# Performance work log

Hardware: AMD Instinct MI355X
Metric: run time of the kernel (lower is better)

## Reference

```python
import jax, jax.numpy as jnp
import numpy as np

LEAKY_SLOPE = 0.01  # torch F.leaky_relu default
COS_EPS = 1e-8      # torch F.cosine_similarity default eps


def _gc(pre, cur, adj, W):
    # GraphConvolution.forward
    pre_w = pre @ W            # [N, d]
    cur_w = cur @ W            # [M, d]
    new_pre = adj @ cur_w      # [N, d]
    new_cur = adj.T @ pre_w    # [M, d]
    new_pre = jnp.where(new_pre >= 0, new_pre, LEAKY_SLOPE * new_pre)
    new_cur = jnp.where(new_cur >= 0, new_cur, LEAKY_SLOPE * new_cur)
    return new_pre, new_cur


def _cos_sim(pre, cur):
    # Fused pairwise cosine similarity: matches torch F.cosine_similarity per pair
    dots = pre @ cur.T                         # [N, M]
    n_pre = jnp.linalg.norm(pre, axis=1)       # [N]
    n_cur = jnp.linalg.norm(cur, axis=1)       # [M]
    denom = jnp.maximum(n_pre[:, None] * n_cur[None, :], COS_EPS)
    return dots / denom


def setup_inputs() -> dict:
    key = jax.random.key(0)
    k1, k2, k3, k4, k5 = jax.random.split(key, 5)
    N, d = 8192, 128
    stdv = 1.0 / np.sqrt(d)
    pre = jax.random.normal(k1, (N, d), dtype=jnp.float32)
    cur = jax.random.normal(k2, (N, d), dtype=jnp.float32)
    adj = jax.random.uniform(k3, (N, N), dtype=jnp.float32)
    W1 = jax.random.uniform(k4, (d, d), dtype=jnp.float32, minval=-stdv, maxval=stdv)
    W2 = jax.random.uniform(k5, (d, d), dtype=jnp.float32, minval=-stdv, maxval=stdv)
    return {"pre": pre, "cur": cur, "adj": adj, "W1": W1, "W2": W2}


def reference(pre, cur, adj, W1, W2):
    pre1, cur1 = _gc(pre, cur, adj, W1)
    adj1 = _cos_sim(pre1, cur1)
    pre2, cur2 = _gc(pre1, cur1, adj1, W2)
    adj2 = _cos_sim(pre2, cur2)
    return adj2
```

## Files before the change

kernel.cpp:

```cpp
#include <hip/hip_runtime.h>


#define NN 8192
#define DD 128

typedef __bf16 bf16x8 __attribute__((ext_vector_type(8)));
typedef float f32x4 __attribute__((ext_vector_type(4)));

static __device__ __forceinline__ float4 ldg4(const float* p) {
    return *reinterpret_cast<const float4*>(p);
}

static __device__ __forceinline__ unsigned f2bf2(float lo, float hi) {
    __bf16 a = (__bf16)lo, b = (__bf16)hi;
    unsigned short ua = __builtin_bit_cast(unsigned short, a);
    unsigned short ub = __builtin_bit_cast(unsigned short, b);
    return (unsigned)ua | ((unsigned)ub << 16);
}

static __device__ __forceinline__ int swz16(int row) {
    return (((row & 7) ^ ((row >> 3) & 7)) << 4);
}

template<int AMODE>
__global__ __launch_bounds__(256, 4)
void mfma_tn(const void* __restrict__ Aptr, int lda,
             const unsigned short* __restrict__ BTa,
             const unsigned short* __restrict__ BTb, int ldbt,
             float* __restrict__ C, int ldc,
             int ksplit, int zstride)
{
    __shared__ alignas(16) char smem[34816];
    char* smA = smem;
    char* smB = smem + 16384;

    const int t    = threadIdx.x;
    const int l    = t & 63;
    const int w    = t >> 6;
    const int wr   = (w >> 1) * 64;
    const int wc   = (w & 1) * 64;
    const int lrow = l & 15;
    const int lhi  = l >> 4;
    const int i0   = blockIdx.x * 128;
    const int j0   = blockIdx.y * 128;
    const int z    = blockIdx.z;
    const bool second = (AMODE == 3) && (z >= 8);
    const unsigned short* BT = second ? BTb : BTa;
    const int kbase = (AMODE == 3) ? (z & 7) * ksplit : 0;
    C += (size_t)z * (size_t)zstride;

    const int srow = t >> 3;
    const int skg  = t & 7;
    const int u    = t & 31;
    const int r8   = t >> 5;

    f32x4 acc[4][4];
    #pragma unroll
    for (int r = 0; r < 4; ++r)
        #pragma unroll
        for (int q = 0; q < 4; ++q)
            #pragma unroll
            for (int e = 0; e < 4; ++e) acc[r][q][e] = 0.0f;

    for (int k0 = 0; k0 < ksplit; k0 += 64) {
        const int kk = kbase + k0;

        if (AMODE == 3 && second) {
            const float* gA = (const float*)Aptr;
            float4 rv[8];
            #pragma unroll
            for (int e = 0; e < 8; ++e)
                rv[e] = ldg4(&gA[(size_t)(kk + r8 * 8 + e) * lda + i0 + u * 4]);
            {
                int c = u * 4;
                uint4 wv;
                wv.x = f2bf2(rv[0].x, rv[1].x); wv.y = f2bf2(rv[2].x, rv[3].x);
                wv.z = f2bf2(rv[4].x, rv[5].x); wv.w = f2bf2(rv[6].x, rv[7].x);
                *reinterpret_cast<uint4*>(smA + c * 128 + ((r8 << 4) ^ swz16(c))) = wv;
                c = u * 4 + 1;
                wv.x = f2bf2(rv[0].y, rv[1].y); wv.y = f2bf2(rv[2].y, rv[3].y);
                wv.z = f2bf2(rv[4].y, rv[5].y); wv.w = f2bf2(rv[6].y, rv[7].y);
                *reinterpret_cast<uint4*>(smA + c * 128 + ((r8 << 4) ^ swz16(c))) = wv;
                c = u * 4 + 2;
                wv.x = f2bf2(rv[0].z, rv[1].z); wv.y = f2bf2(rv[2].z, rv[3].z);
                wv.z = f2bf2(rv[4].z, rv[5].z); wv.w = f2bf2(rv[6].z, rv[7].z);
                *reinterpret_cast<uint4*>(smA + c * 128 + ((r8 << 4) ^ swz16(c))) = wv;
                c = u * 4 + 3;
                wv.x = f2bf2(rv[0].w, rv[1].w); wv.y = f2bf2(rv[2].w, rv[3].w);
                wv.z = f2bf2(rv[4].w, rv[5].w); wv.w = f2bf2(rv[6].w, rv[7].w);
                *reinterpret_cast<uint4*>(smA + c * 128 + ((r8 << 4) ^ swz16(c))) = wv;
            }
        } else {
            #pragma unroll
            for (int it = 0; it < 4; ++it) {
                const int row = it * 32 + srow;
                const int dst = row * 128 + ((skg << 4) ^ swz16(row));
                if constexpr (AMODE == 3) {
                    const float* g = (const float*)Aptr + (size_t)(i0 + row) * lda + kk + skg * 8;
                    float4 f0 = ldg4(g), f1 = ldg4(g + 4);
                    uint4 wv;
                    wv.x = f2bf2(f0.x, f0.y);
                    wv.y = f2bf2(f0.z, f0.w);
                    wv.z = f2bf2(f1.x, f1.y);
                    wv.w = f2bf2(f1.z, f1.w);
                    *reinterpret_cast<uint4*>(smA + dst) = wv;
                } else {
                    const unsigned short* g = (const unsigned short*)Aptr + (size_t)(i0 + row) * lda + kk + skg * 8;
                    *reinterpret_cast<uint4*>(smA + dst) = *reinterpret_cast<const uint4*>(g);
                }
            }
        }

        #pragma unroll
        for (int it = 0; it < 4; ++it) {
            const int row = it * 32 + srow;
            const int dst = row * 128 + ((skg << 4) ^ swz16(row));
            const unsigned short* gb = BT + (size_t)(j0 + it * 32 + srow) * ldbt + kk + skg * 8;
            *reinterpret_cast<uint4*>(smB + dst) = *reinterpret_cast<const uint4*>(gb);
        }
        __syncthreads();

        #pragma unroll
        for (int s = 0; s < 2; ++s) {
            bf16x8 af[4], bq[4];
            #pragma unroll
            for (int r = 0; r < 4; ++r) {
                const int row = wr + r * 16 + lrow;
                af[r] = *reinterpret_cast<const bf16x8*>(
                    smA + row * 128 + ((s * 64 + lhi * 16) ^ swz16(row)));
            }
            #pragma unroll
            for (int q = 0; q < 4; ++q) {
                const int col = wc + q * 16 + lrow;
                bq[q] = *reinterpret_cast<const bf16x8*>(
                    smB + col * 128 + ((s * 64 + lhi * 16) ^ swz16(col)));
            }
            #pragma unroll
            for (int r = 0; r < 4; ++r)
                #pragma unroll
                for (int q = 0; q < 4; ++q)
                    acc[r][q] = __builtin_amdgcn_mfma_f32_16x16x32_bf16(af[r], bq[q], acc[r][q], 0, 0, 0);
        }
        __syncthreads();
    }

    float* sC = (float*)smem;
    #pragma unroll
    for (int h = 0; h < 2; ++h) {
        if ((w & 1) == h) {
            #pragma unroll
            for (int r = 0; r < 4; ++r)
                #pragma unroll
                for (int q = 0; q < 4; ++q)
                    #pragma unroll
                    for (int i = 0; i < 4; ++i)
                        sC[(wr + r * 16 + lhi * 4 + i) * 68 + q * 16 + lrow] = acc[r][q][i];
        }
        __syncthreads();
        #pragma unroll
        for (int it = 0; it < 8; ++it) {
            const int idx = it * 256 + t;
            const int row = idx >> 4;
            const int c4  = (idx & 15) << 2;
            f32x4 v = *reinterpret_cast<const f32x4*>(&sC[row * 68 + c4]);
            float* dst = &C[(size_t)(i0 + row) * ldc + j0 + h * 64 + c4];
            if constexpr (AMODE == 0)
                __builtin_nontemporal_store(v, reinterpret_cast<f32x4*>(dst));
            else
                *reinterpret_cast<f32x4*>(dst) = v;
        }
        __syncthreads();
    }
}

__global__ __launch_bounds__(256, 2)
void gemm_w1t(const float* __restrict__ pre, const float* __restrict__ cur,
              const float* __restrict__ W1,
              unsigned short* __restrict__ pwT, unsigned short* __restrict__ cwT)
{
    __shared__ float sA[32][68];
    __shared__ float sB[64][128];

    const int t  = threadIdx.x;
    const int ct = t & 31;
    const int rt = t >> 5;
    const int bx = blockIdx.x;
    const bool isCur = bx >= 256;
    const float* A = isCur ? cur : pre;
    unsigned short* XT = isCur ? cwT : pwT;
    const int i0 = (bx & 255) * 32;

    float4 acc[4];
    #pragma unroll
    for (int r = 0; r < 4; ++r) { acc[r].x = 0.f; acc[r].y = 0.f; acc[r].z = 0.f; acc[r].w = 0.f; }

    for (int k0 = 0; k0 < DD; k0 += 64) {
        #pragma unroll
        for (int f = 0; f < 2; ++f) {
            const int row = (t >> 4) + 16 * f;
            const int kk4 = (t & 15) << 2;
            *reinterpret_cast<float4*>(&sA[row][kk4]) =
                ldg4(&A[(size_t)(i0 + row) * DD + k0 + kk4]);
        }
        #pragma unroll
        for (int f = 0; f < 8; ++f) {
            const int idx = f * 256 + t;
            const int kk  = idx >> 5;
            const int c4  = (idx & 31) << 2;
            *reinterpret_cast<float4*>(&sB[kk][c4]) =
                ldg4(&W1[(size_t)(k0 + kk) * DD + c4]);
        }
        __syncthreads();
        #pragma unroll 4
        for (int kk = 0; kk < 64; kk += 4) {
            float4 a[4], b[4];
            #pragma unroll
            for (int r = 0; r < 4; ++r)
                a[r] = *reinterpret_cast<const float4*>(&sA[rt * 4 + r][kk]);
            #pragma unroll
            for (int q = 0; q < 4; ++q)
                b[q] = *reinterpret_cast<const float4*>(&sB[kk + q][ct * 4]);
            #pragma unroll
            for (int r = 0; r < 4; ++r) {
                acc[r].x += a[r].x * b[0].x; acc[r].y += a[r].x * b[0].y;
                acc[r].z += a[r].x * b[0].z; acc[r].w += a[r].x * b[0].w;
                acc[r].x += a[r].y * b[1].x; acc[r].y += a[r].y * b[1].y;
                acc[r].z += a[r].y * b[1].z; acc[r].w += a[r].y * b[1].w;
                acc[r].x += a[r].z * b[2].x; acc[r].y += a[r].z * b[2].y;
                acc[r].z += a[r].z * b[2].z; acc[r].w += a[r].z * b[2].w;
                acc[r].x += a[r].w * b[3].x; acc[r].y += a[r].w * b[3].y;
                acc[r].z += a[r].w * b[3].z; acc[r].w += a[r].w * b[3].w;
            }
        }
        __syncthreads();
    }

    float* sC = &sB[0][0];
    #pragma unroll
    for (int r = 0; r < 4; ++r)
        *reinterpret_cast<float4*>(&sC[(rt * 4 + r) * 128 + ct * 4]) = acc[r];
    __syncthreads();

    const int n = t & 127;
    const int g = t >> 7;
    #pragma unroll
    for (int c = 0; c < 2; ++c) {
        const int ii = (2 * g + c) * 8;
        uint4 wv;
        wv.x = f2bf2(sC[(ii + 0) * 128 + n], sC[(ii + 1) * 128 + n]);
        wv.y = f2bf2(sC[(ii + 2) * 128 + n], sC[(ii + 3) * 128 + n]);
        wv.z = f2bf2(sC[(ii + 4) * 128 + n], sC[(ii + 5) * 128 + n]);
        wv.w = f2bf2(sC[(ii + 6) * 128 + n], sC[(ii + 7) * 128 + n]);
        *reinterpret_cast<uint4*>(&XT[(size_t)n * NN + i0 + ii]) = wv;
    }
}

__global__ __launch_bounds__(128)
void rln(const float* __restrict__ kparts, float* __restrict__ Xbase,
         float* __restrict__ invbase)
{
    const int i = blockIdx.x;
    const int y = blockIdx.y;
    const int t = threadIdx.x;
    const float* part = kparts + (size_t)(1 - y) * 8 * (NN * DD);
    float* X = Xbase + (size_t)y * (NN * DD);
    float* inv_n = invbase + y * NN;

    float s = 0.f;
    #pragma unroll
    for (int z = 0; z < 8; ++z)
        s += part[(size_t)z * (NN * DD) + (size_t)i * DD + t];
    float y_ = (s >= 0.f) ? s : 0.01f * s;
    X[(size_t)i * DD + t] = y_;
    float n = y_ * y_;
    #pragma unroll
    for (int o = 32; o > 0; o >>= 1) n += __shfl_down(n, o);
    __shared__ float p[2];
    if ((t & 63) == 0) p[t >> 6] = n;
    __syncthreads();
    if (t == 0) inv_n[i] = 1.0f / sqrtf(p[0] + p[1]);
}

template<bool TRANSA, bool SCALEK, int EPI>
__global__ __launch_bounds__(256, 2)
void gemm32(const float* __restrict__ A, int lda,
            const float* __restrict__ B, int ldb,
            float* __restrict__ C, unsigned short* __restrict__ Cb,
            int ksplit_len, int zstride,
            const float* __restrict__ kscale,
            const float* __restrict__ rscale,
            int ystA, int ystB, int ystC, int ystS)
{
    __shared__ float sA[32][68];
    __shared__ float sB[64][128];

    const int t  = threadIdx.x;
    const int ct = t & 31;
    const int rt = t >> 5;
    const int i0 = blockIdx.x * 32;
    const int side = blockIdx.y;
    const int kgbase = blockIdx.z * ksplit_len;

    A += (ptrdiff_t)side * ystA;
    B += (ptrdiff_t)side * ystB;
    if constexpr (EPI == 0)
        C += (ptrdiff_t)side * ystC + (size_t)blockIdx.z * (size_t)zstride;
    if constexpr (EPI == 3)
        Cb += (ptrdiff_t)side * ystC;
    if constexpr (SCALEK) kscale += (ptrdiff_t)side * ystS;
    if constexpr (EPI == 3) rscale += (ptrdiff_t)side * ystS;

    float4 acc[4];
    #pragma unroll
    for (int r = 0; r < 4; ++r) { acc[r].x = 0.f; acc[r].y = 0.f; acc[r].z = 0.f; acc[r].w = 0.f; }

    for (int k0 = 0; k0 < ksplit_len; k0 += 64) {
        const int kg = kgbase + k0;
        if (!TRANSA) {
            #pragma unroll
            for (int f = 0; f < 2; ++f) {
                const int row = (t >> 4) + 16 * f;
                const int kk4 = (t & 15) << 2;
                *reinterpret_cast<float4*>(&sA[row][kk4]) =
                    ldg4(&A[(size_t)(i0 + row) * lda + kg + kk4]);
            }
        } else {
            #pragma unroll
            for (int f = 0; f < 2; ++f) {
                const int kk = (t >> 3) + 32 * f;
                const int r4 = (t & 7) << 2;
                float4 v = ldg4(&A[(size_t)(kg + kk) * lda + i0 + r4]);
                if (SCALEK) {
                    const float s = kscale[kg + kk];
                    v.x *= s; v.y *= s; v.z *= s; v.w *= s;
                }
                sA[r4 + 0][kk] = v.x; sA[r4 + 1][kk] = v.y;
                sA[r4 + 2][kk] = v.z; sA[r4 + 3][kk] = v.w;
            }
        }
        #pragma unroll
        for (int f = 0; f < 8; ++f) {
            const int idx = f * 256 + t;
            const int kk  = idx >> 5;
            const int c4  = (idx & 31) << 2;
            *reinterpret_cast<float4*>(&sB[kk][c4]) =
                ldg4(&B[(size_t)(kg + kk) * ldb + c4]);
        }
        __syncthreads();
        #pragma unroll 4
        for (int kk = 0; kk < 64; kk += 4) {
            float4 a[4], b[4];
            #pragma unroll
            for (int r = 0; r < 4; ++r)
                a[r] = *reinterpret_cast<const float4*>(&sA[rt * 4 + r][kk]);
            #pragma unroll
            for (int q = 0; q < 4; ++q)
                b[q] = *reinterpret_cast<const float4*>(&sB[kk + q][ct * 4]);
            #pragma unroll
            for (int r = 0; r < 4; ++r) {
                acc[r].x += a[r].x * b[0].x; acc[r].y += a[r].x * b[0].y;
                acc[r].z += a[r].x * b[0].z; acc[r].w += a[r].x * b[0].w;
                acc[r].x += a[r].y * b[1].x; acc[r].y += a[r].y * b[1].y;
                acc[r].z += a[r].y * b[1].z; acc[r].w += a[r].y * b[1].w;
                acc[r].x += a[r].z * b[2].x; acc[r].y += a[r].z * b[2].y;
                acc[r].z += a[r].z * b[2].z; acc[r].w += a[r].z * b[2].w;
                acc[r].x += a[r].w * b[3].x; acc[r].y += a[r].w * b[3].y;
                acc[r].z += a[r].w * b[3].z; acc[r].w += a[r].w * b[3].w;
            }
        }
        __syncthreads();
    }

    #pragma unroll
    for (int r = 0; r < 4; ++r) {
        const int rg = i0 + rt * 4 + r;
        if constexpr (EPI == 3) {
            const float s = rscale[rg];
            float y0 = acc[r].x * s, y1 = acc[r].y * s,
                  y2 = acc[r].z * s, y3 = acc[r].w * s;
            y0 = (y0 >= 0.f) ? y0 : 0.01f * y0;
            y1 = (y1 >= 0.f) ? y1 : 0.01f * y1;
            y2 = (y2 >= 0.f) ? y2 : 0.01f * y2;
            y3 = (y3 >= 0.f) ? y3 : 0.01f * y3;
            float ss = y0 * y0 + y1 * y1 + y2 * y2 + y3 * y3;
            #pragma unroll
            for (int m = 16; m > 0; m >>= 1) ss += __shfl_xor(ss, m);
            const float invn = rsqrtf(ss);
            uint2 wv;
            wv.x = f2bf2(y0 * invn, y1 * invn);
            wv.y = f2bf2(y2 * invn, y3 * invn);
            *reinterpret_cast<uint2*>(&Cb[(size_t)rg * DD + ct * 4]) = wv;
        } else {
            *reinterpret_cast<float4*>(&C[(size_t)rg * DD + ct * 4]) = acc[r];
        }
    }
}

__global__ __launch_bounds__(256)
void reduce_mcmp(const float* __restrict__ part, float* __restrict__ out)
{
    const int y = blockIdx.y;
    const int i = blockIdx.x * 256 + threadIdx.x;
    part += (size_t)y * 32 * 16384;
    out  += (size_t)y * 16384;
    float a = 0.f;
    #pragma unroll
    for (int z = 0; z < 32; ++z) a += part[(size_t)z * 16384 + i];
    out[i] = a;
}

extern "C" void kernel_launch(void* const* d_in, const int* in_sizes, int n_in,
                              void* d_out, int out_size, void* d_ws, size_t ws_size,
                              hipStream_t stream)
{
    const float* pre = (const float*)d_in[0];
    const float* cur = (const float*)d_in[1];
    const float* adj = (const float*)d_in[2];
    const float* W1  = (const float*)d_in[3];
    const float* W2  = (const float*)d_in[4];
    float* out = (float*)d_out;
    float* ws  = (float*)d_ws;

    const size_t M1 = (size_t)NN * DD;

    float* cwpw2 = ws + 0 * M1;
    float* c1    = ws + 2 * M1;
    unsigned short* c2n_b = (unsigned short*)(ws + 4 * M1);
    unsigned short* p2n_b = c2n_b + M1;
    unsigned short* cwT_b = (unsigned short*)(ws + 5 * M1);
    unsigned short* pwT_b = cwT_b + M1;
    float* bparts = ws + 6 * M1;
    float* mcmp   = ws + 7 * M1;
    float* inc1   = mcmp + 32768;
    float* kparts = ws + 8 * M1;

    gemm_w1t<<<dim3(512,1,1),256,0,stream>>>(pre, cur, W1, pwT_b, cwT_b);

    mfma_tn<3><<<dim3(64,1,16),256,0,stream>>>(adj, NN, cwT_b, pwT_b, NN,
                                               kparts, DD, NN/8, (int)M1);

    rln<<<dim3(NN,2,1),128,0,stream>>>(kparts, c1, inc1);

    gemm32<false,false,0><<<dim3(512,1,1),256,0,stream>>>(
        c1, DD, W2, DD, cwpw2, (unsigned short*)nullptr,
        DD, 0, nullptr, nullptr, 0,0,0,0);

    gemm32<true,true,0><<<dim3(4,2,32),256,0,stream>>>(
        c1, DD, cwpw2, DD, bparts, (unsigned short*)nullptr,
        256, 16384, inc1, nullptr,
        (int)M1, (int)M1, 32*16384, NN);

    reduce_mcmp<<<dim3(64,2,1),256,0,stream>>>(bparts, mcmp);

    gemm32<false,false,3><<<dim3(256,2,1),256,0,stream>>>(
        c1, DD, mcmp + 16384, DD, (float*)nullptr, c2n_b,
        DD, 0, nullptr, inc1,
        (int)M1, -16384, (int)M1, NN);

    mfma_tn<0><<<dim3(64,64,1),256,0,stream>>>(p2n_b, DD, c2n_b, c2n_b, DD,
                                               out, NN, DD, 0);
}
```

Before: 284.6 us.

## Double-buffer LDS in MFMA GEMM with register prefetch and halve K-split

Rewrites the mfma_tn main loop into a two-stage software pipeline: global loads for the next K tile are issued into registers while MFMAs run on the current LDS buffer, using two LDS buffers and explicit vmcnt waits and barriers. The K-split for the first adjacency GEMM is reduced from 8 to 4 partitions, with the grid and the rln reduction changed to match. This is meant to hide global-load latency and cut partial-sum traffic, but LDS use doubles and launch bounds drop to 2 blocks per SM, so occupancy falls and the grid has half as many blocks.

```diff
diff --git a/kernel.cpp b/kernel.cpp
--- a/kernel.cpp
+++ b/kernel.cpp
@@ -18,21 +18,23 @@
     return (unsigned)ua | ((unsigned)ub << 16);
 }
 
+#define FC(v, j) ((j) == 0 ? (v).x : (j) == 1 ? (v).y : (j) == 2 ? (v).z : (v).w)
+
 static __device__ __forceinline__ int swz16(int row) {
     return (((row & 7) ^ ((row >> 3) & 7)) << 4);
 }
 
+#define PRAGU _Pragma("unroll")
+
 template<int AMODE>
-__global__ __launch_bounds__(256, 4)
+__global__ __launch_bounds__(256, 2)
 void mfma_tn(const void* __restrict__ Aptr, int lda,
              const unsigned short* __restrict__ BTa,
              const unsigned short* __restrict__ BTb, int ldbt,
              float* __restrict__ C, int ldc,
              int ksplit, int zstride)
 {
-    __shared__ alignas(16) char smem[34816];
-    char* smA = smem;
-    char* smB = smem + 16384;
+    __shared__ alignas(16) char smem[65536];
 
     const int t    = threadIdx.x;
     const int l    = t & 63;
@@ -44,9 +46,9 @@
     const int i0   = blockIdx.x * 128;
     const int j0   = blockIdx.y * 128;
     const int z    = blockIdx.z;
-    const bool second = (AMODE == 3) && (z >= 8);
+    const bool second = (AMODE == 3) && (z >= 4);
     const unsigned short* BT = second ? BTb : BTa;
-    const int kbase = (AMODE == 3) ? (z & 7) * ksplit : 0;
+    const int kbase = (AMODE == 3) ? (z & 3) * ksplit : 0;
     C += (size_t)z * (size_t)zstride;
 
     const int srow = t >> 3;
@@ -55,109 +57,156 @@
     const int r8   = t >> 5;
 
     f32x4 acc[4][4];
-    #pragma unroll
+    PRAGU
     for (int r = 0; r < 4; ++r)
-        #pragma unroll
+        PRAGU
         for (int q = 0; q < 4; ++q)
-            #pragma unroll
+            PRAGU
             for (int e = 0; e < 4; ++e) acc[r][q][e] = 0.0f;
 
-    for (int k0 = 0; k0 < ksplit; k0 += 64) {
-        const int kk = kbase + k0;
-
-        if (AMODE == 3 && second) {
-            const float* gA = (const float*)Aptr;
-            float4 rv[8];
-            #pragma unroll
-            for (int e = 0; e < 8; ++e)
-                rv[e] = ldg4(&gA[(size_t)(kk + r8 * 8 + e) * lda + i0 + u * 4]);
-            {
-                int c = u * 4;
-                uint4 wv;
-                wv.x = f2bf2(rv[0].x, rv[1].x); wv.y = f2bf2(rv[2].x, rv[3].x);
-                wv.z = f2bf2(rv[4].x, rv[5].x); wv.w = f2bf2(rv[6].x, rv[7].x);
-                *reinterpret_cast<uint4*>(smA + c * 128 + ((r8 << 4) ^ swz16(c))) = wv;
-                c = u * 4 + 1;
-                wv.x = f2bf2(rv[0].y, rv[1].y); wv.y = f2bf2(rv[2].y, rv[3].y);
-                wv.z = f2bf2(rv[4].y, rv[5].y); wv.w = f2bf2(rv[6].y, rv[7].y);
-                *reinterpret_cast<uint4*>(smA + c * 128 + ((r8 << 4) ^ swz16(c))) = wv;
-                c = u * 4 + 2;
-                wv.x = f2bf2(rv[0].z, rv[1].z); wv.y = f2bf2(rv[2].z, rv[3].z);
-                wv.z = f2bf2(rv[4].z, rv[5].z); wv.w = f2bf2(rv[6].z, rv[7].z);
-                *reinterpret_cast<uint4*>(smA + c * 128 + ((r8 << 4) ^ swz16(c))) = wv;
-                c = u * 4 + 3;
-                wv.x = f2bf2(rv[0].w, rv[1].w); wv.y = f2bf2(rv[2].w, rv[3].w);
-                wv.z = f2bf2(rv[4].w, rv[5].w); wv.w = f2bf2(rv[6].w, rv[7].w);
-                *reinterpret_cast<uint4*>(smA + c * 128 + ((r8 << 4) ^ swz16(c))) = wv;
-            }
-        } else {
-            #pragma unroll
-            for (int it = 0; it < 4; ++it) {
-                const int row = it * 32 + srow;
-                const int dst = row * 128 + ((skg << 4) ^ swz16(row));
-                if constexpr (AMODE == 3) {
-                    const float* g = (const float*)Aptr + (size_t)(i0 + row) * lda + kk + skg * 8;
-                    float4 f0 = ldg4(g), f1 = ldg4(g + 4);
-                    uint4 wv;
-                    wv.x = f2bf2(f0.x, f0.y);
-                    wv.y = f2bf2(f0.z, f0.w);
-                    wv.z = f2bf2(f1.x, f1.y);
-                    wv.w = f2bf2(f1.z, f1.w);
-                    *reinterpret_cast<uint4*>(smA + dst) = wv;
-                } else {
-                    const unsigned short* g = (const unsigned short*)Aptr + (size_t)(i0 + row) * lda + kk + skg * 8;
-                    *reinterpret_cast<uint4*>(smA + dst) = *reinterpret_cast<const uint4*>(g);
-                }
-            }
-        }
-
-        #pragma unroll
-        for (int it = 0; it < 4; ++it) {
-            const int row = it * 32 + srow;
-            const int dst = row * 128 + ((skg << 4) ^ swz16(row));
-            const unsigned short* gb = BT + (size_t)(j0 + it * 32 + srow) * ldbt + kk + skg * 8;
-            *reinterpret_cast<uint4*>(smB + dst) = *reinterpret_cast<const uint4*>(gb);
-        }
-        __syncthreads();
-
-        #pragma unroll
+    float4 faA[8], faB[8];
+    uint4  uaA[4], uaB[4];
+    uint4  ubA[4], ubB[4];
+
+#define LOADM(kk_, fa_, ua_, ub_)                                              \
+    do {                                                                       \
+        const int kk__ = (kk_);                                                \
+        if constexpr (AMODE == 3) {                                            \
+            if (second) {                                                      \
+                const float* gA_ = (const float*)Aptr;                         \
+                PRAGU for (int e = 0; e < 8; ++e)                              \
+                    fa_[e] = ldg4(&gA_[(size_t)(kk__ + r8 * 8 + e) * lda + i0 + u * 4]); \
+            } else {                                                           \
+                PRAGU for (int it = 0; it < 4; ++it) {                         \
+                    const float* g_ = (const float*)Aptr +                     \
+                        (size_t)(i0 + it * 32 + srow) * lda + kk__ + skg * 8;  \
+                    fa_[2 * it] = ldg4(g_); fa_[2 * it + 1] = ldg4(g_ + 4);    \
+                }                                                              \
+            }                                                                  \
+        } else {                                                               \
+            PRAGU for (int it = 0; it < 4; ++it)                               \
+                ua_[it] = *reinterpret_cast<const uint4*>(                     \
+                    (const unsigned short*)Aptr +                              \
+                    (size_t)(i0 + it * 32 + srow) * lda + kk__ + skg * 8);     \
+        }                                                                      \
+        PRAGU for (int it = 0; it < 4; ++it)                                   \
+            ub_[it] = *reinterpret_cast<const uint4*>(                         \
+                BT + (size_t)(j0 + it * 32 + srow) * ldbt + kk__ + skg * 8);   \
+    } while (0)
+
+#define WRITEM(buf_, fa_, ua_, ub_)                                            \
+    do {                                                                       \
+        char* smA_ = smem + (buf_) * 32768;                                    \
+        char* smB_ = smA_ + 16384;                                             \
+        if constexpr (AMODE == 3) {                                            \
+            if (second) {                                                      \
+                PRAGU for (int j = 0; j < 4; ++j) {                            \
+                    const int c_ = u * 4 + j;                                  \
+                    uint4 wv_;                                                 \
+                    wv_.x = f2bf2(FC(fa_[0], j), FC(fa_[1], j));               \
+                    wv_.y = f2bf2(FC(fa_[2], j), FC(fa_[3], j));               \
+                    wv_.z = f2bf2(FC(fa_[4], j), FC(fa_[5], j));               \
+                    wv_.w = f2bf2(FC(fa_[6], j), FC(fa_[7], j));               \
+                    *reinterpret_cast<uint4*>(smA_ + c_ * 128 + ((r8 << 4) ^ swz16(c_))) = wv_; \
+                }                                                              \
+            } else {                                                           \
+                PRAGU for (int it = 0; it < 4; ++it) {                         \
+                    const int row_ = it * 32 + srow;                           \
+                    uint4 wv_;                                                 \
+                    wv_.x = f2bf2(fa_[2 * it].x, fa_[2 * it].y);               \
+                    wv_.y = f2bf2(fa_[2 * it].z, fa_[2 * it].w);               \
+                    wv_.z = f2bf2(fa_[2 * it + 1].x, fa_[2 * it + 1].y);       \
+                    wv_.w = f2bf2(fa_[2 * it + 1].z, fa_[2 * it + 1].w);       \
+                    *reinterpret_cast<uint4*>(smA_ + row_ * 128 + ((skg << 4) ^ swz16(row_))) = wv_; \
+                }                                                              \
+            }                                                                  \
+        } else {                                                               \
+            PRAGU for (int it = 0; it < 4; ++it) {                             \
+                const int row_ = it * 32 + srow;                               \
+                *reinterpret_cast<uint4*>(smA_ + row_ * 128 + ((skg << 4) ^ swz16(row_))) = ua_[it]; \
+            }                                                                  \
+        }                                                                      \
+        PRAGU for (int it = 0; it < 4; ++it) {                                 \
+            const int row_ = it * 32 + srow;                                   \
+            *reinterpret_cast<uint4*>(smB_ + row_ * 128 + ((skg << 4) ^ swz16(row_))) = ub_[it]; \
+        }                                                                      \
+    } while (0)
+
+#define WAITNV()                                                               \
+    do { if constexpr (AMODE == 3)                                             \
+             asm volatile("s_waitcnt vmcnt(12)" ::: "memory");                 \
+         else                                                                  \
+             asm volatile("s_waitcnt vmcnt(8)" ::: "memory"); } while (0)
+#define WAIT0() asm volatile("s_waitcnt vmcnt(0)" ::: "memory")
+
+#define BARRIER()                                                              \
+    do { asm volatile("s_waitcnt lgkmcnt(0)" ::: "memory");                    \
+         __builtin_amdgcn_s_barrier();                                         \
+         __builtin_amdgcn_sched_barrier(0); } while (0)
+
+    auto MFMA_STEP = [&](const int buf) {
+        char* smA = smem + buf * 32768;
+        char* smB = smA + 16384;
+        PRAGU
         for (int s = 0; s < 2; ++s) {
             bf16x8 af[4], bq[4];
-            #pragma unroll
+            PRAGU
             for (int r = 0; r < 4; ++r) {
                 const int row = wr + r * 16 + lrow;
                 af[r] = *reinterpret_cast<const bf16x8*>(
                     smA + row * 128 + ((s * 64 + lhi * 16) ^ swz16(row)));
             }
-            #pragma unroll
+            PRAGU
             for (int q = 0; q < 4; ++q) {
                 const int col = wc + q * 16 + lrow;
                 bq[q] = *reinterpret_cast<const bf16x8*>(
                     smB + col * 128 + ((s * 64 + lhi * 16) ^ swz16(col)));
             }
-            #pragma unroll
+            PRAGU
             for (int r = 0; r < 4; ++r)
-                #pragma unroll
+                PRAGU
                 for (int q = 0; q < 4; ++q)
                     acc[r][q] = __builtin_amdgcn_mfma_f32_16x16x32_bf16(af[r], bq[q], acc[r][q], 0, 0, 0);
         }
-        __syncthreads();
+    };
+
+    const int nt = ksplit >> 6;
+    LOADM(kbase, faA, uaA, ubA);
+    LOADM(kbase + 64, faB, uaB, ubB);
+    WAITNV();
+    WRITEM(0, faA, uaA, ubA);
+    BARRIER();
+
+    for (int tt = 0; tt < nt; tt += 2) {
+        MFMA_STEP(0);
+        if (tt + 2 < nt) { LOADM(kbase + (tt + 2) * 64, faA, uaA, ubA); WAITNV(); }
+        else             { WAIT0(); }
+        WRITEM(1, faB, uaB, ubB);
+        BARRIER();
+        MFMA_STEP(1);
+        if (tt + 2 < nt) {
+            LOADM(kbase + (tt + 3) * 64, faB, uaB, ubB);
+            WAITNV();
+            WRITEM(0, faA, uaA, ubA);
+            BARRIER();
+        }
     }
+    __syncthreads();
 
     float* sC = (float*)smem;
-    #pragma unroll
+    PRAGU
     for (int h = 0; h < 2; ++h) {
         if ((w & 1) == h) {
-            #pragma unroll
+            PRAGU
             for (int r = 0; r < 4; ++r)
-                #pragma unroll
+                PRAGU
                 for (int q = 0; q < 4; ++q)
-                    #pragma unroll
+                    PRAGU
                     for (int i = 0; i < 4; ++i)
                         sC[(wr + r * 16 + lhi * 4 + i) * 68 + q * 16 + lrow] = acc[r][q][i];
         }
         __syncthreads();
-        #pragma unroll
+        PRAGU
         for (int it = 0; it < 8; ++it) {
             const int idx = it * 256 + t;
             const int row = idx >> 4;
@@ -171,6 +220,11 @@
         }
         __syncthreads();
     }
+#undef LOADM
+#undef WRITEM
+#undef WAITNV
+#undef WAIT0
+#undef BARRIER
 }
 
 __global__ __launch_bounds__(256, 2)
@@ -262,13 +316,13 @@
     const int i = blockIdx.x;
     const int y = blockIdx.y;
     const int t = threadIdx.x;
-    const float* part = kparts + (size_t)(1 - y) * 8 * (NN * DD);
+    const float* part = kparts + (size_t)(1 - y) * 4 * (NN * DD);
     float* X = Xbase + (size_t)y * (NN * DD);
     float* inv_n = invbase + y * NN;
 
     float s = 0.f;
     #pragma unroll
-    for (int z = 0; z < 8; ++z)
+    for (int z = 0; z < 4; ++z)
         s += part[(size_t)z * (NN * DD) + (size_t)i * DD + t];
     float y_ = (s >= 0.f) ? s : 0.01f * s;
     X[(size_t)i * DD + t] = y_;
@@ -436,8 +490,8 @@
 
     gemm_w1t<<<dim3(512,1,1),256,0,stream>>>(pre, cur, W1, pwT_b, cwT_b);
 
-    mfma_tn<3><<<dim3(64,1,16),256,0,stream>>>(adj, NN, cwT_b, pwT_b, NN,
-                                               kparts, DD, NN/8, (int)M1);
+    mfma_tn<3><<<dim3(64,1,8),256,0,stream>>>(adj, NN, cwT_b, pwT_b, NN,
+                                              kparts, DD, NN/4, (int)M1);
 
     rln<<<dim3(NN,2,1),128,0,stream>>>(kparts, c1, inc1);
 
```

Measured after the change: 362.5 us. +27.4%, slower.
